# Performance work log

Hardware: AMD Instinct MI355X
Metric: run time of the kernel (lower is better)

The kernel has to match this reference:

```python
import jax, jax.numpy as jnp
import numpy as np

N = 729        # problem variables
B = 8          # batch
K = 32         # mixing rank (hard-coded in MixingFunc)
NB = 40        # number of symmetry-basis matrices
MAX_ITER = 10  # coordinate-descent sweeps


def setup_inputs() -> dict:
    key = jax.random.key(0)
    ks = jax.random.split(key, 7)
    coeff = jax.random.normal(ks[0], (NB,), jnp.float32)
    upper = jax.random.normal(ks[1], (N,), jnp.float32)
    basis = jax.random.normal(ks[2], (NB, N, N), jnp.float32)
    z = jax.random.uniform(ks[3], (B, N), jnp.float32)
    is_input = jax.random.randint(ks[4], (B, N), 0, 2).astype(jnp.int32)
    v_init_raw = jax.random.normal(ks[5], (B, N + 1, K), jnp.float32)
    # random permutation of the N non-truth variables (indices 1..N), as in satnet init
    perm = (jax.random.permutation(ks[6], N) + 1).astype(jnp.int32)
    return dict(coeff=coeff, upper=upper, basis=basis, z=z,
                is_input=is_input, v_init_raw=v_init_raw, perm=perm)


def _build_C(coeff, upper, basis):
    # BasisFunc.forward: C = [[0, upper^T], [upper, sum_b coeff_b * basis_b]]
    center = jnp.einsum('b,bij->ij', coeff, basis)              # (N, N)
    top = jnp.concatenate([jnp.zeros((1,), upper.dtype), upper])[None, :]  # (1, N+1)
    bottom = jnp.concatenate([upper[:, None], center], axis=1)  # (N, N+1)
    return jnp.concatenate([top, bottom], axis=0)               # (N+1, N+1)


def _init_V(v_raw, z_full):
    # SATNet init: v0 = random unit truth direction; each v_i is placed on the
    # cone around v0 at angle pi*z_i using a random orthogonal direction.
    v0 = v_raw[:, 0] / jnp.linalg.norm(v_raw[:, 0], axis=-1, keepdims=True)  # (B, K)
    dot = jnp.einsum('bnk,bk->bn', v_raw, v0)
    u = v_raw - dot[..., None] * v0[:, None, :]
    u = u / jnp.maximum(jnp.linalg.norm(u, axis=-1, keepdims=True), 1e-8)
    c = jnp.cos(jnp.pi * z_full)[..., None]
    s = jnp.sin(jnp.pi * z_full)[..., None]
    V = -c * v0[:, None, :] + s * u                              # (B, N+1, K)
    V = V.at[:, 0].set(v0)                                       # truth vector pinned
    return V


def _mix(C, V, is_input_full, perm):
    # SATNet mixing coordinate descent: for each free variable i,
    #   g_i = sum_j C[j,i] v_j - C[i,i] v_i ;  v_i <- -g_i / ||g_i||
    Cdiag = jnp.diagonal(C)
    free = (is_input_full == 0)                                  # (B, N+1)

    def coord_step(V, i):
        g = jnp.einsum('j,bjk->bk', C[:, i], V) - Cdiag[i] * V[:, i]  # (B, K)
        gn = jnp.linalg.norm(g, axis=-1, keepdims=True)
        vnew = -g / jnp.maximum(gn, 1e-8)
        V = V.at[:, i].set(jnp.where(free[:, i][:, None], vnew, V[:, i]))
        return V, None

    def sweep(V, _):
        V, _ = jax.lax.scan(coord_step, V, perm)
        return V, None

    V, _ = jax.lax.scan(jax.checkpoint(sweep), V, None, length=MAX_ITER)
    return V


def reference(coeff, upper, basis, z, is_input, v_init_raw, perm):
    Bn = z.shape[0]
    C = _build_C(coeff, upper, basis)
    z_full = jnp.concatenate([jnp.ones((Bn, 1), z.dtype), z], axis=1)
    ii_full = jnp.concatenate(
        [jnp.ones((Bn, 1), is_input.dtype), is_input], axis=1)
    V = _init_V(v_init_raw, z_full)
    V = _mix(C, V, ii_full, perm)
    v0 = V[:, 0]
    cosang = jnp.clip(-jnp.einsum('bnk,bk->bn', V, v0), -1.0 + 1e-6, 1.0 - 1e-6)
    zo = jnp.arccos(cosang) / jnp.pi
    z_out = jnp.where(ii_full == 1, z_full, zo)
    return z_out[:, 1:]
```

## Files before the change

kernel.cpp:

```cpp
#include <hip/hip_runtime.h>

#define NN   729
#define NF   730
#define BV   8
#define KK   32
#define NBAS 40
#define MAXIT 10
#define PI_F 3.14159265358979323846f

#define MTH   512
#define BT    16
#define AST   448

typedef float v2f __attribute__((ext_vector_type(2)));

__device__ __forceinline__ void fma4(float4& w, float c, const float4& d) {
    w.x = fmaf(c, d.x, w.x); w.y = fmaf(c, d.y, w.y);
    w.z = fmaf(c, d.z, w.z); w.w = fmaf(c, d.w, w.w);
}

__global__ void build_C_kernel(const float* __restrict__ coeff,
                               const float* __restrict__ upper,
                               const float* __restrict__ basis,
                               float* __restrict__ Ct) {
    int idx = blockIdx.x * blockDim.x + threadIdx.x;
    if (idx >= NF * NF) return;
    int i = idx / NF, j = idx - i * NF;
    float val;
    if (i == 0) {
        val = (j == 0) ? 0.f : upper[j - 1];
    } else if (j == 0) {
        val = upper[i - 1];
    } else {
        float acc = 0.f;
        const float* bp = basis + (size_t)(i - 1) * NN + (j - 1);
        #pragma unroll 8
        for (int b = 0; b < NBAS; ++b)
            acc = fmaf(coeff[b], bp[(size_t)b * NN * NN], acc);
        val = acc;
    }
    Ct[(size_t)j * NF + i] = val;
}

__global__ void init_V_kernel(const float* __restrict__ z,
                              const float* __restrict__ vraw,
                              float* __restrict__ V) {
    int g = threadIdx.x >> 5;
    int k = threadIdx.x & 31;
    int row = blockIdx.x * 8 + g;
    int b = row / NF, n = row - b * NF;
    const float* vr = vraw + (size_t)b * NF * KK;

    float v0 = vr[k];
    float s2 = v0 * v0;
    #pragma unroll
    for (int off = 16; off; off >>= 1) s2 += __shfl_xor(s2, off, 32);
    v0 = v0 / sqrtf(s2);

    float vn = vr[(size_t)n * KK + k];
    float d = vn * v0;
    #pragma unroll
    for (int off = 16; off; off >>= 1) d += __shfl_xor(d, off, 32);
    float u = vn - d * v0;
    float un2 = u * u;
    #pragma unroll
    for (int off = 16; off; off >>= 1) un2 += __shfl_xor(un2, off, 32);
    u = u / fmaxf(sqrtf(un2), 1e-8f);

    float zf = (n == 0) ? 1.f : z[b * NN + (n - 1)];
    float c = cosf(PI_F * zf), s = sinf(PI_F * zf);
    float outv = -c * v0 + s * u;
    if (n == 0) outv = v0;
    V[((size_t)b * NF + n) * KK + k] = outv;
}

__global__ void build_act_kernel(const int* __restrict__ is_input,
                                 const int* __restrict__ perm,
                                 int* __restrict__ act, int* __restrict__ nA_arr) {
    int b = blockIdx.x, l = threadIdx.x;
    int base = 0;
    for (int c = 0; c < (NN + 63) / 64; ++c) {
        int idx = c * 64 + l;
        bool f = false; int pi = 0;
        if (idx < NN) { pi = perm[idx]; f = (is_input[b * NN + pi - 1] == 0); }
        unsigned long long m = __ballot(f);
        int pos = __popcll(m & ((1ull << l) - 1ull));
        if (f && base + pos < AST) act[b * AST + base + pos] = pi;
        base += __popcll(m);
    }
    if (base > AST) base = AST;
    if (l == 0) nA_arr[b] = base;
    for (int p = base + l; p < AST; p += 64) act[b * AST + p] = 0;
}

__global__ void gather_CactT_kernel(const float* __restrict__ Ct,
                                    const int* __restrict__ act,
                                    float* __restrict__ CactT) {
    int a = blockIdx.x, b = blockIdx.y;
    __shared__ int acts[AST];
    for (int i = threadIdx.x; i < AST; i += blockDim.x) acts[i] = act[b * AST + i];
    __syncthreads();
    const float* src = Ct + (size_t)acts[a] * NF;
    float* dst = CactT + ((size_t)b * AST + a) * AST;
    for (int t = threadIdx.x; t < AST; t += blockDim.x)
        dst[t] = src[acts[t]];
}

__global__ void init_W_kernel(const float* __restrict__ Ct,
                              const int* __restrict__ act,
                              const int* __restrict__ nA_arr,
                              const float* __restrict__ V,
                              float* __restrict__ Wc,
                              float* __restrict__ Vact) {
    int b = blockIdx.y;
    int a = blockIdx.x * 8 + (threadIdx.x >> 5);
    int k = threadIdx.x & 31;
    int nA = nA_arr[b];
    float w = 0.f;
    int ra = act[b * AST + a];
    float vv = V[((size_t)b * NF + ra) * KK + k];
    if (a < nA) {
        const float* ctr = Ct + (size_t)ra * NF;
        const float* vb = V + (size_t)b * NF * KK + k;
        float acc = 0.f;
        for (int j = 0; j < NF; ++j)
            acc = fmaf(ctr[j], vb[(size_t)j * KK], acc);
        w = acc - ctr[ra] * vv;
    }
    Wc[((size_t)b * AST + a) * KK + k] = w;
    Vact[((size_t)b * AST + a) * KK + k] = vv;
}

__device__ __forceinline__ float rowsum16(float x) {
    int y;
    y = __builtin_amdgcn_update_dpp(0, __float_as_int(x), 0x121, 0xF, 0xF, false);
    x += __int_as_float(y);
    y = __builtin_amdgcn_update_dpp(0, __float_as_int(x), 0x122, 0xF, 0xF, false);
    x += __int_as_float(y);
    y = __builtin_amdgcn_update_dpp(0, __float_as_int(x), 0x124, 0xF, 0xF, false);
    x += __int_as_float(y);
    y = __builtin_amdgcn_update_dpp(0, __float_as_int(x), 0x128, 0xF, 0xF, false);
    x += __int_as_float(y);
    return x;
}

__global__ __launch_bounds__(MTH, 2)
void mix_kernel(const float* __restrict__ CactT_g,
                const float* __restrict__ Wc_g,
                const float* __restrict__ Vact_g,
                const int* __restrict__ act_g,
                const int* __restrict__ nA_arr,
                const int* __restrict__ is_input,
                const float* __restrict__ z,
                const float* __restrict__ Vg,
                float* __restrict__ out) {
    __shared__ __align__(16) float V_c[AST * KK];
    __shared__ __align__(16) float dv_s[2][BT * KK];
    __shared__ __align__(16) float gpub[2][BT * KK];
    __shared__ __align__(16) float cblk_s[2][BT * BT];
    __shared__ __align__(16) float cmini_s[BT * BT];
    __shared__ float Cd_s[AST];
    __shared__ int   slot_s[NF];

    int b = blockIdx.x, tid = threadIdx.x;
    const float* CT = CactT_g + (size_t)b * AST * AST;
    const float* Vact = Vact_g + (size_t)b * AST * KK;
    int nA = nA_arr[b];
    int nblkp = (nA + BT - 1) / BT;
    if (nblkp < 2) nblkp = 2;
    int nAp = nblkp * BT;
    int totB = MAXIT * nblkp;

    int wid = tid >> 6;
    int l64 = tid & 63;
    int lane = tid - 64;
    int kq = lane & 7;
    int rslot = lane >> 3;
    int k32 = tid & 31;

    for (int idx = tid; idx < AST * 8; idx += MTH)
        ((float4*)V_c)[idx] = ((const float4*)Vact)[idx];
    if (tid < AST) Cd_s[tid] = CT[(size_t)tid * AST + tid];
    if (tid < nA) slot_s[act_g[b * AST + tid]] = tid;
    if (tid < 256) {
        int t = tid >> 4, u = tid & 15;
        cblk_s[0][t * BT + u] = CT[(size_t)u * AST + t];
    }
    float4 w[8];
    #pragma unroll
    for (int p = 0; p < 8; ++p) {
        float4 zz = {0.f, 0.f, 0.f, 0.f};
        w[p] = zz;
        if (wid >= 1)
            w[p] = *(const float4*)&Wc_g[((size_t)b * AST + rslot + 56 * p) * KK + 4 * kq];
    }
    if (wid >= 1) {
        #pragma unroll
        for (int p = 0; p < 8; ++p) {
            int a = rslot + 56 * p;
            if ((a >> 4) == 0)
                *(float4*)&gpub[1][a * KK + 4 * kq] = w[p];
        }
    }
    __syncthreads();

    for (int bi = 0; bi < totB; ++bi) {
        int blk = bi % nblkp, s0 = blk * BT;
        int pblk = (bi - 1 + nblkp) % nblkp, sp0 = pblk * BT;
        int cb = bi & 1, pv = cb ^ 1;
        int nblk2 = (bi + 1) % nblkp, sn0 = nblk2 * BT;

        if (wid == 0) {
            __builtin_amdgcn_s_setprio(1);
            float g[BT], vo[BT];
            #pragma unroll
            for (int u = 0; u < BT; ++u) {
                g[u]  = gpub[pv][u * KK + k32];
                vo[u] = V_c[(s0 + u) * KK + k32];
            }
            #pragma unroll
            for (int u = 0; u < BT; ++u) {
                int s = s0 + u;
                float n2 = g[u] * g[u];
                n2 = rowsum16(n2);
                n2 += __shfl_xor(n2, 16, 32);
                float inv = -__builtin_amdgcn_rsqf(fmaxf(n2, 1e-16f));
                float msk = (s < nA) ? 1.f : 0.f;
                float d = fmaf(g[u], inv, -vo[u]) * msk;
                if (tid < 32) {
                    dv_s[cb][u * KK + k32] = d;
                    V_c[s * KK + k32] = vo[u] + d;
                }
                #pragma unroll
                for (int u2 = u + 1; u2 < BT; ++u2)
                    g[u2] = fmaf(cblk_s[cb][u * BT + u2], d, g[u2]);
            }
            __builtin_amdgcn_s_setprio(0);
        } else {
            if (wid == 6) {
                int u = l64 & 15, q = l64 >> 4;
                float4 v = *(const float4*)&CT[(size_t)(sn0 + u) * AST + s0 + 4 * q];
                *(float4*)&cmini_s[u * BT + 4 * q] = v;
            }
            if (wid == 7) {
                int u = l64 & 15, q = l64 >> 4;
                float4 v = *(const float4*)&CT[(size_t)(sn0 + u) * AST + sn0 + 4 * q];
                cblk_s[pv][(4 * q + 0) * BT + u] = v.x;
                cblk_s[pv][(4 * q + 1) * BT + u] = v.y;
                cblk_s[pv][(4 * q + 2) * BT + u] = v.z;
                cblk_s[pv][(4 * q + 3) * BT + u] = v.w;
            }
            if (bi > 0) {
                #pragma unroll
                for (int h = 0; h < 2; ++h) {
                    float4 dvv[8];
                    #pragma unroll
                    for (int t = 0; t < 8; ++t)
                        dvv[t] = *(const float4*)&dv_s[pv][(8 * h + t) * KK + 4 * kq];
                    float4 cA0, cB0, cA1, cB1;
                    {
                        const float* cr = CT + (size_t)rslot * AST + sp0 + 8 * h;
                        cA0 = *(const float4*)(cr);
                        cB0 = *(const float4*)(cr + 4);
                    }
                    #pragma unroll
                    for (int p = 0; p < 8; ++p) {
                        int a = rslot + 56 * p;
                        if (p < 7) {
                            const float* cr = CT + (size_t)(a + 56) * AST + sp0 + 8 * h;
                            if (p & 1) { cA0 = *(const float4*)(cr); cB0 = *(const float4*)(cr + 4); }
                            else       { cA1 = *(const float4*)(cr); cB1 = *(const float4*)(cr + 4); }
                        }
                        float4 ca = (p & 1) ? cA1 : cA0;
                        float4 cbq = (p & 1) ? cB1 : cB0;
                        if (a < nAp) {
                            fma4(w[p], ca.x,  dvv[0]);
                            fma4(w[p], ca.y,  dvv[1]);
                            fma4(w[p], ca.z,  dvv[2]);
                            fma4(w[p], ca.w,  dvv[3]);
                            fma4(w[p], cbq.x, dvv[4]);
                            fma4(w[p], cbq.y, dvv[5]);
                            fma4(w[p], cbq.z, dvv[6]);
                            fma4(w[p], cbq.w, dvv[7]);
                        }
                    }
                }
                #pragma unroll
                for (int p = 0; p < 8; ++p) {
                    int a = rslot + 56 * p;
                    if ((a >> 4) == pblk) {
                        float4 dd = *(const float4*)&dv_s[pv][(a - sp0) * KK + 4 * kq];
                        fma4(w[p], -Cd_s[a], dd);
                    }
                }
            }
            #pragma unroll
            for (int p = 0; p < 8; ++p) {
                int a = rslot + 56 * p;
                if ((a >> 4) == nblk2)
                    *(float4*)&gpub[cb][(a - sn0) * KK + 4 * kq] = w[p];
            }
        }
        __syncthreads();

        {
            int u = tid >> 5, k = tid & 31;
            float g = gpub[cb][u * KK + k];
            #pragma unroll
            for (int t = 0; t < BT; ++t)
                g = fmaf(cmini_s[u * BT + t], dv_s[cb][t * KK + k], g);
            gpub[cb][u * KK + k] = g;
        }
        __syncthreads();
    }

    int k = tid & 31, r = tid >> 5;
    float v0k = Vg[(size_t)b * NF * KK + k];
    for (int n = 1 + r; n <= NN; n += 16) {
        int ii = is_input[b * NN + n - 1];
        float res;
        if (ii == 1) {
            res = z[b * NN + n - 1];
        } else {
            int a = slot_s[n];
            float dot = V_c[a * KK + k] * v0k;
            #pragma unroll
            for (int off = 16; off; off >>= 1) dot += __shfl_xor(dot, off, 32);
            float ca = fminf(fmaxf(-dot, -1.f + 1e-6f), 1.f - 1e-6f);
            res = acosf(ca) * (1.f / PI_F);
        }
        if (k == 0) out[b * NN + n - 1] = res;
    }
}

extern "C" void kernel_launch(void* const* d_in, const int* in_sizes, int n_in,
                              void* d_out, int out_size, void* d_ws, size_t ws_size,
                              hipStream_t stream) {
    const float* coeff    = (const float*)d_in[0];
    const float* upper    = (const float*)d_in[1];
    const float* basis    = (const float*)d_in[2];
    const float* z        = (const float*)d_in[3];
    const int*   is_input = (const int*)d_in[4];
    const float* vraw     = (const float*)d_in[5];
    const int*   perm     = (const int*)d_in[6];
    float* out = (float*)d_out;

    float* ws    = (float*)d_ws;
    float* Ct    = ws;
    float* V     = Ct + (size_t)NF * NF;
    float* CactT = V + (size_t)BV * NF * KK;
    float* Wc    = CactT + (size_t)BV * AST * AST;
    float* Vact  = Wc + (size_t)BV * AST * KK;
    int*   act   = (int*)(Vact + (size_t)BV * AST * KK);
    int*   nAa   = act + BV * AST;

    build_C_kernel<<<dim3((NF * NF + 255) / 256), dim3(256), 0, stream>>>(coeff, upper, basis, Ct);
    init_V_kernel<<<dim3(730), dim3(256), 0, stream>>>(z, vraw, V);
    build_act_kernel<<<dim3(BV), dim3(64), 0, stream>>>(is_input, perm, act, nAa);
    gather_CactT_kernel<<<dim3(AST, BV), dim3(256), 0, stream>>>(Ct, act, CactT);
    init_W_kernel<<<dim3(AST / 8, BV), dim3(256), 0, stream>>>(Ct, act, nAa, V, Wc, Vact);
    mix_kernel<<<dim3(BV), dim3(MTH), 0, stream>>>(CactT, Wc, Vact, act, nAa, is_input, z, V, out);
}
```

Measured before the change: 744.1 us.

## Use bf16 MFMA for block gradient update with prepacked C fragments

Replaces the fp32 FMA rank-16 update of the gradient accumulators in the mix kernel with bf16 16x16x32 MFMA instructions, keeping accumulators in MFMA output layout. A new prepack kernel gathers active rows/cols of C into bf16 fragment layout per 16x16 tile, replacing the fp32 CactT gather; mini-blocks for the sequential part are now gathered directly from C via act indices. This aims to cut the per-step ALU and memory cost of the bulk update, at the price of bf16 rounding error accumulating over ten sweeps, and half-idle MFMA (K padded from 16 to 32).

```diff
diff --git a/kernel.cpp b/kernel.cpp
--- a/kernel.cpp
+++ b/kernel.cpp
@@ -11,12 +11,15 @@
 #define MTH   512
 #define BT    16
 #define AST   448
-
-typedef float v2f __attribute__((ext_vector_type(2)));
-
-__device__ __forceinline__ void fma4(float4& w, float c, const float4& d) {
-    w.x = fmaf(c, d.x, w.x); w.y = fmaf(c, d.y, w.y);
-    w.z = fmaf(c, d.z, w.z); w.w = fmaf(c, d.w, w.w);
+#define NMT   28
+
+typedef short v8s __attribute__((ext_vector_type(8)));
+typedef float v4f __attribute__((ext_vector_type(4)));
+
+__device__ __forceinline__ unsigned short f2bf(float f) {
+    unsigned int x = __float_as_uint(f);
+    unsigned int r = x + 0x7FFFu + ((x >> 16) & 1u);
+    return (unsigned short)(r >> 16);
 }
 
 __global__ void build_C_kernel(const float* __restrict__ coeff,
@@ -91,19 +94,6 @@
     if (base > AST) base = AST;
     if (l == 0) nA_arr[b] = base;
     for (int p = base + l; p < AST; p += 64) act[b * AST + p] = 0;
-}
-
-__global__ void gather_CactT_kernel(const float* __restrict__ Ct,
-                                    const int* __restrict__ act,
-                                    float* __restrict__ CactT) {
-    int a = blockIdx.x, b = blockIdx.y;
-    __shared__ int acts[AST];
-    for (int i = threadIdx.x; i < AST; i += blockDim.x) acts[i] = act[b * AST + i];
-    __syncthreads();
-    const float* src = Ct + (size_t)acts[a] * NF;
-    float* dst = CactT + ((size_t)b * AST + a) * AST;
-    for (int t = threadIdx.x; t < AST; t += blockDim.x)
-        dst[t] = src[acts[t]];
 }
 
 __global__ void init_W_kernel(const float* __restrict__ Ct,
@@ -131,6 +121,26 @@
     Vact[((size_t)b * AST + a) * KK + k] = vv;
 }
 
+__global__ void prepack_A_kernel(const float* __restrict__ Ct,
+                                 const int* __restrict__ act,
+                                 v8s* __restrict__ Apack) {
+    int b = blockIdx.y, pm = blockIdx.x;
+    int pb = pm / NMT, mt = pm - NMT * pb;
+    int l = threadIdx.x;
+    if (l >= 32) return;
+    int row = mt * 16 + (l & 15);
+    int ra = act[b * AST + row];
+    const float* crow = Ct + (size_t)ra * NF;
+    v8s v;
+    #pragma unroll
+    for (int i = 0; i < 8; ++i) {
+        int t = (l >> 4) * 8 + i;
+        int rt = act[b * AST + pb * 16 + t];
+        v[i] = (short)f2bf(crow[rt]);
+    }
+    Apack[(((size_t)b * NMT + pb) * NMT + mt) * 32 + l] = v;
+}
+
 __device__ __forceinline__ float rowsum16(float x) {
     int y;
     y = __builtin_amdgcn_update_dpp(0, __float_as_int(x), 0x121, 0xF, 0xF, false);
@@ -145,7 +155,8 @@
 }
 
 __global__ __launch_bounds__(MTH, 2)
-void mix_kernel(const float* __restrict__ CactT_g,
+void mix_kernel(const v8s* __restrict__ Apack_g,
+                const float* __restrict__ Ct_g,
                 const float* __restrict__ Wc_g,
                 const float* __restrict__ Vact_g,
                 const int* __restrict__ act_g,
@@ -161,45 +172,57 @@
     __shared__ __align__(16) float cmini_s[BT * BT];
     __shared__ float Cd_s[AST];
     __shared__ int   slot_s[NF];
+    __shared__ int   act_s[AST];
 
     int b = blockIdx.x, tid = threadIdx.x;
-    const float* CT = CactT_g + (size_t)b * AST * AST;
+    const v8s* Apack = Apack_g + ((size_t)b * NMT * NMT) * 32;
     const float* Vact = Vact_g + (size_t)b * AST * KK;
     int nA = nA_arr[b];
     int nblkp = (nA + BT - 1) / BT;
     if (nblkp < 2) nblkp = 2;
-    int nAp = nblkp * BT;
+    if (nblkp > NMT) nblkp = NMT;
     int totB = MAXIT * nblkp;
 
     int wid = tid >> 6;
     int l64 = tid & 63;
-    int lane = tid - 64;
-    int kq = lane & 7;
-    int rslot = lane >> 3;
+    int col = l64 & 15, rg = l64 >> 4;
     int k32 = tid & 31;
 
+    if (tid < AST) act_s[tid] = act_g[b * AST + tid];
+    __syncthreads();
     for (int idx = tid; idx < AST * 8; idx += MTH)
         ((float4*)V_c)[idx] = ((const float4*)Vact)[idx];
-    if (tid < AST) Cd_s[tid] = CT[(size_t)tid * AST + tid];
-    if (tid < nA) slot_s[act_g[b * AST + tid]] = tid;
+    if (tid < AST) Cd_s[tid] = Ct_g[(size_t)act_s[tid] * NF + act_s[tid]];
+    if (tid < nA) slot_s[act_s[tid]] = tid;
     if (tid < 256) {
         int t = tid >> 4, u = tid & 15;
-        cblk_s[0][t * BT + u] = CT[(size_t)u * AST + t];
-    }
-    float4 w[8];
-    #pragma unroll
-    for (int p = 0; p < 8; ++p) {
-        float4 zz = {0.f, 0.f, 0.f, 0.f};
-        w[p] = zz;
-        if (wid >= 1)
-            w[p] = *(const float4*)&Wc_g[((size_t)b * AST + rslot + 56 * p) * KK + 4 * kq];
-    }
+        cblk_s[0][t * BT + u] = Ct_g[(size_t)act_s[u] * NF + act_s[t]];
+    }
+    v4f acc[4][2];
+    #pragma unroll
+    for (int tl = 0; tl < 4; ++tl)
+        #pragma unroll
+        for (int nt = 0; nt < 2; ++nt) {
+            v4f z4 = {0.f, 0.f, 0.f, 0.f};
+            acc[tl][nt] = z4;
+        }
     if (wid >= 1) {
         #pragma unroll
-        for (int p = 0; p < 8; ++p) {
-            int a = rslot + 56 * p;
-            if ((a >> 4) == 0)
-                *(float4*)&gpub[1][a * KK + 4 * kq] = w[p];
+        for (int tl = 0; tl < 4; ++tl) {
+            int mt = (wid - 1) * 4 + tl;
+            #pragma unroll
+            for (int nt = 0; nt < 2; ++nt)
+                #pragma unroll
+                for (int i = 0; i < 4; ++i)
+                    acc[tl][nt][i] =
+                        Wc_g[((size_t)b * AST + mt * 16 + rg * 4 + i) * KK + nt * 16 + col];
+        }
+        if (wid == 1) {
+            #pragma unroll
+            for (int nt = 0; nt < 2; ++nt)
+                #pragma unroll
+                for (int i = 0; i < 4; ++i)
+                    gpub[1][(rg * 4 + i) * KK + nt * 16 + col] = acc[0][nt][i];
         }
     }
     __syncthreads();
@@ -238,67 +261,64 @@
             __builtin_amdgcn_s_setprio(0);
         } else {
             if (wid == 6) {
-                int u = l64 & 15, q = l64 >> 4;
-                float4 v = *(const float4*)&CT[(size_t)(sn0 + u) * AST + s0 + 4 * q];
-                *(float4*)&cmini_s[u * BT + 4 * q] = v;
+                for (int idx = l64; idx < BT * BT; idx += 64) {
+                    int u = idx >> 4, t = idx & 15;
+                    cmini_s[u * BT + t] =
+                        Ct_g[(size_t)act_s[sn0 + u] * NF + act_s[s0 + t]];
+                }
             }
             if (wid == 7) {
-                int u = l64 & 15, q = l64 >> 4;
-                float4 v = *(const float4*)&CT[(size_t)(sn0 + u) * AST + sn0 + 4 * q];
-                cblk_s[pv][(4 * q + 0) * BT + u] = v.x;
-                cblk_s[pv][(4 * q + 1) * BT + u] = v.y;
-                cblk_s[pv][(4 * q + 2) * BT + u] = v.z;
-                cblk_s[pv][(4 * q + 3) * BT + u] = v.w;
+                for (int idx = l64; idx < BT * BT; idx += 64) {
+                    int x = idx >> 4, y = idx & 15;
+                    cblk_s[pv][idx] =
+                        Ct_g[(size_t)act_s[sn0 + y] * NF + act_s[sn0 + x]];
+                }
             }
             if (bi > 0) {
-                #pragma unroll
-                for (int h = 0; h < 2; ++h) {
-                    float4 dvv[8];
+                v8s bf0, bf1;
+                #pragma unroll
+                for (int i = 0; i < 8; ++i) { bf0[i] = 0; bf1[i] = 0; }
+                if (l64 < 32) {
                     #pragma unroll
-                    for (int t = 0; t < 8; ++t)
-                        dvv[t] = *(const float4*)&dv_s[pv][(8 * h + t) * KK + 4 * kq];
-                    float4 cA0, cB0, cA1, cB1;
-                    {
-                        const float* cr = CT + (size_t)rslot * AST + sp0 + 8 * h;
-                        cA0 = *(const float4*)(cr);
-                        cB0 = *(const float4*)(cr + 4);
+                    for (int i = 0; i < 8; ++i) {
+                        int t = rg * 8 + i;
+                        bf0[i] = (short)f2bf(dv_s[pv][t * KK + col]);
+                        bf1[i] = (short)f2bf(dv_s[pv][t * KK + 16 + col]);
                     }
+                }
+                #pragma unroll
+                for (int tl = 0; tl < 4; ++tl) {
+                    int mt = (wid - 1) * 4 + tl;
+                    v8s af;
                     #pragma unroll
-                    for (int p = 0; p < 8; ++p) {
-                        int a = rslot + 56 * p;
-                        if (p < 7) {
-                            const float* cr = CT + (size_t)(a + 56) * AST + sp0 + 8 * h;
-                            if (p & 1) { cA0 = *(const float4*)(cr); cB0 = *(const float4*)(cr + 4); }
-                            else       { cA1 = *(const float4*)(cr); cB1 = *(const float4*)(cr + 4); }
-                        }
-                        float4 ca = (p & 1) ? cA1 : cA0;
-                        float4 cbq = (p & 1) ? cB1 : cB0;
-                        if (a < nAp) {
-                            fma4(w[p], ca.x,  dvv[0]);
-                            fma4(w[p], ca.y,  dvv[1]);
-                            fma4(w[p], ca.z,  dvv[2]);
-                            fma4(w[p], ca.w,  dvv[3]);
-                            fma4(w[p], cbq.x, dvv[4]);
-                            fma4(w[p], cbq.y, dvv[5]);
-                            fma4(w[p], cbq.z, dvv[6]);
-                            fma4(w[p], cbq.w, dvv[7]);
+                    for (int i = 0; i < 8; ++i) af[i] = 0;
+                    if (l64 < 32)
+                        af = Apack[((size_t)pblk * NMT + mt) * 32 + l64];
+                    acc[tl][0] = __builtin_amdgcn_mfma_f32_16x16x32_bf16(af, bf0, acc[tl][0], 0, 0, 0);
+                    acc[tl][1] = __builtin_amdgcn_mfma_f32_16x16x32_bf16(af, bf1, acc[tl][1], 0, 0, 0);
+                }
+                #pragma unroll
+                for (int tl = 0; tl < 4; ++tl) {
+                    if ((wid - 1) * 4 + tl == pblk) {
+                        #pragma unroll
+                        for (int i = 0; i < 4; ++i) {
+                            int r = rg * 4 + i;
+                            float cd = Cd_s[sp0 + r];
+                            acc[tl][0][i] = fmaf(-cd, dv_s[pv][r * KK + col],      acc[tl][0][i]);
+                            acc[tl][1][i] = fmaf(-cd, dv_s[pv][r * KK + 16 + col], acc[tl][1][i]);
                         }
                     }
                 }
-                #pragma unroll
-                for (int p = 0; p < 8; ++p) {
-                    int a = rslot + 56 * p;
-                    if ((a >> 4) == pblk) {
-                        float4 dd = *(const float4*)&dv_s[pv][(a - sp0) * KK + 4 * kq];
-                        fma4(w[p], -Cd_s[a], dd);
+            }
+            #pragma unroll
+            for (int tl = 0; tl < 4; ++tl) {
+                if ((wid - 1) * 4 + tl == nblk2) {
+                    #pragma unroll
+                    for (int i = 0; i < 4; ++i) {
+                        gpub[cb][(rg * 4 + i) * KK + col]      = acc[tl][0][i];
+                        gpub[cb][(rg * 4 + i) * KK + 16 + col] = acc[tl][1][i];
                     }
                 }
-            }
-            #pragma unroll
-            for (int p = 0; p < 8; ++p) {
-                int a = rslot + 56 * p;
-                if ((a >> 4) == nblk2)
-                    *(float4*)&gpub[cb][(a - sn0) * KK + 4 * kq] = w[p];
             }
         }
         __syncthreads();
@@ -345,19 +365,19 @@
     const int*   perm     = (const int*)d_in[6];
     float* out = (float*)d_out;
 
-    float* ws    = (float*)d_ws;
-    float* Ct    = ws;
-    float* V     = Ct + (size_t)NF * NF;
-    float* CactT = V + (size_t)BV * NF * KK;
-    float* Wc    = CactT + (size_t)BV * AST * AST;
-    float* Vact  = Wc + (size_t)BV * AST * KK;
-    int*   act   = (int*)(Vact + (size_t)BV * AST * KK);
-    int*   nAa   = act + BV * AST;
+    float* ws   = (float*)d_ws;
+    float* Ct   = ws;
+    float* V    = Ct + (size_t)NF * NF;
+    float* Wc   = V + (size_t)BV * NF * KK;
+    float* Vact = Wc + (size_t)BV * AST * KK;
+    int*   act  = (int*)(Vact + (size_t)BV * AST * KK);
+    int*   nAa  = act + BV * AST;
+    v8s*  Apack = (v8s*)(nAa + 8);
 
     build_C_kernel<<<dim3((NF * NF + 255) / 256), dim3(256), 0, stream>>>(coeff, upper, basis, Ct);
     init_V_kernel<<<dim3(730), dim3(256), 0, stream>>>(z, vraw, V);
     build_act_kernel<<<dim3(BV), dim3(64), 0, stream>>>(is_input, perm, act, nAa);
-    gather_CactT_kernel<<<dim3(AST, BV), dim3(256), 0, stream>>>(Ct, act, CactT);
     init_W_kernel<<<dim3(AST / 8, BV), dim3(256), 0, stream>>>(Ct, act, nAa, V, Wc, Vact);
-    mix_kernel<<<dim3(BV), dim3(MTH), 0, stream>>>(CactT, Wc, Vact, act, nAa, is_input, z, V, out);
-}
+    prepack_A_kernel<<<dim3(NMT * NMT, BV), dim3(64), 0, stream>>>(Ct, act, Apack);
+    mix_kernel<<<dim3(BV), dim3(MTH), 0, stream>>>(Apack, Ct, Wc, Vact, act, nAa, is_input, z, V, out);
+}
```

New measurement: 722.5 us (median of 2 runs). -2.9%, faster.
